# Performance work log

Measured on AMD Instinct MI355X. Metric: run time of the kernel, lower is better.

Reference implementation:

```python
import jax, jax.numpy as jnp
import numpy as np

N_NODES = 4096
D_FEAT = 256


def _interp_linear_2x(x):
    # Matches F.interpolate(mode='linear', scale_factor=2, align_corners=False)
    # applied along the node axis. x: [N, D] -> [2N, D]
    n = x.shape[0]
    out_i = jnp.arange(2 * n, dtype=jnp.float32)
    src = jnp.clip((out_i + 0.5) * 0.5 - 0.5, 0.0, float(n - 1))
    i0 = jnp.floor(src).astype(jnp.int32)
    i1 = jnp.minimum(i0 + 1, n - 1)
    w = (src - i0.astype(jnp.float32))[:, None]
    return x[i0] * (1.0 - w) + x[i1] * w


def _nearest_neighbor_idx(x):
    # argmin over pairwise Euclidean distances with diagonal excluded.
    # Squared distances give the same argmin as torch.cdist.
    sq = jnp.sum(x * x, axis=1)
    d2 = sq[:, None] + sq[None, :] - 2.0 * (x @ x.T)  # [2N, 2N]
    m = x.shape[0]
    d2 = jnp.where(jnp.eye(m, dtype=bool), jnp.inf, d2)
    return jnp.argmin(d2, axis=1)


def setup_inputs() -> dict:
    key = jax.random.key(0)
    k1, k2, k3, k4 = jax.random.split(key, 4)
    x = jax.random.normal(k1, (N_NODES, D_FEAT), dtype=jnp.float32)
    adj = jax.random.uniform(k2, (N_NODES, N_NODES), dtype=jnp.float32)
    # Xavier-uniform-ish init for the two GCN weights
    lim = float(np.sqrt(6.0 / (D_FEAT + D_FEAT)))
    W1 = jax.random.uniform(k3, (D_FEAT, D_FEAT), jnp.float32, -lim, lim)
    W2 = jax.random.uniform(k4, (D_FEAT, D_FEAT), jnp.float32, -lim, lim)
    return {"x": x, "adj": adj, "W1": W1, "W2": W2}


def reference(x, adj, W1, W2):
    # conv1: adj @ (x @ W1)
    h = adj @ (x @ W1)                      # [N, D]
    x2 = _interp_linear_2x(h)               # [2N, D]
    # nearest-neighbor one-hot adjacency, then conv2.
    # one_hot(nn_idx) @ support == support[nn_idx] (exact same math)
    nn_idx = _nearest_neighbor_idx(x2)      # [2N]
    support = x2 @ W2                       # [2N, D]
    return support[nn_idx]                  # [2N, D]
```

## Files before the change

### kernel.cpp

```cpp
#include <hip/hip_runtime.h>
#include <hip/hip_bf16.h>
#include <cstdint>

typedef __attribute__((ext_vector_type(8))) __bf16 bf16x8;
typedef __attribute__((ext_vector_type(4))) float f32x4;

static __device__ __forceinline__ unsigned short f2bf(float f) {
  return __builtin_bit_cast(unsigned short, (__bf16)f);
}
static __device__ __forceinline__ unsigned pack2(float a, float b) {
  return (unsigned)f2bf(a) | ((unsigned)f2bf(b) << 16);
}
#define GLDS(src, dst) __builtin_amdgcn_global_load_lds( \
    (const __attribute__((address_space(1))) void*)(src), \
    (__attribute__((address_space(3))) void*)(dst), 16, 0, 0)


__global__ void transpose_w_kernel(const float* __restrict__ W1, const float* __restrict__ W2,
                                   unsigned short* __restrict__ W1t, unsigned short* __restrict__ W2t) {
  int i = blockIdx.x * 256 + threadIdx.x;
  int k = i >> 8, n = i & 255;
  W1t[n * 256 + k] = f2bf(W1[k * 256 + n]);
  W2t[n * 256 + k] = f2bf(W2[k * 256 + n]);
}

__global__ void upsample_kernel(const unsigned short* __restrict__ hs,
                                unsigned short* __restrict__ x2b, float* __restrict__ sq) {
  int row = blockIdx.x * 4 + (threadIdx.x >> 6);
  int c = (threadIdx.x & 63) * 4;
  float s = (row + 0.5f) * 0.5f - 0.5f;
  s = fminf(fmaxf(s, 0.0f), 4095.0f);
  float fl = floorf(s);
  int i0 = (int)fl;
  int i1 = min((int)fl + 1, 4095);
  float w = s - fl;
  float v0[4] = {0.f, 0.f, 0.f, 0.f}, v1[4] = {0.f, 0.f, 0.f, 0.f};
  #pragma unroll
  for (int k = 0; k < 8; ++k) {
    ushort4 u0 = *(const ushort4*)&hs[(size_t)k * 4096 * 256 + i0 * 256 + c];
    ushort4 u1 = *(const ushort4*)&hs[(size_t)k * 4096 * 256 + i1 * 256 + c];
    v0[0] += __builtin_bit_cast(float, (unsigned)u0.x << 16);
    v0[1] += __builtin_bit_cast(float, (unsigned)u0.y << 16);
    v0[2] += __builtin_bit_cast(float, (unsigned)u0.z << 16);
    v0[3] += __builtin_bit_cast(float, (unsigned)u0.w << 16);
    v1[0] += __builtin_bit_cast(float, (unsigned)u1.x << 16);
    v1[1] += __builtin_bit_cast(float, (unsigned)u1.y << 16);
    v1[2] += __builtin_bit_cast(float, (unsigned)u1.z << 16);
    v1[3] += __builtin_bit_cast(float, (unsigned)u1.w << 16);
  }
  float p = 0.f;
  ushort4 st;
  unsigned short* sp = (unsigned short*)&st;
  #pragma unroll
  for (int e = 0; e < 4; ++e) {
    float v = v0[e] * (1.0f - w) + v1[e] * w;
    sp[e] = f2bf(v);
    p += v * v;
  }
  *(ushort4*)&x2b[(size_t)row * 256 + c] = st;
  #pragma unroll
  for (int m = 32; m > 0; m >>= 1) p += __shfl_down(p, m, 64);
  if ((threadIdx.x & 63) == 0) sq[row] = p;
}

__global__ void argmin_reduce_kernel(const unsigned* __restrict__ pv,
                                     unsigned* __restrict__ pck) {
  int row = blockIdx.x * 256 + threadIdx.x;
  int cr = row >> 7;
  unsigned best = 0xFFFFFFFFu;
  for (int c = 0; c <= cr; ++c) best = min(best, pv[(size_t)c * 8192 + row]);
  for (int c = cr + 1; c < 64; ++c) best = min(best, pv[(size_t)(64 + c) * 8192 + row]);
  pck[row] = best & 0x1FFFu;
}

__launch_bounds__(256, 3)
__global__ void gram_kernel(const unsigned short* __restrict__ X,
                            const float* __restrict__ sq,
                            unsigned* __restrict__ pv) {
  __shared__ alignas(16) unsigned short As[128 * 64];
  __shared__ alignas(16) unsigned short Bs[128 * 64];
  __shared__ unsigned mrgr[2][128];
  __shared__ unsigned mrgc[2][128];

  const int tid = threadIdx.x;
  const int wid = tid >> 6;
  const int lane = tid & 63;
  const int g = lane >> 4, lr = lane & 15;
  const int wr = wid >> 1, wc = wid & 1;

  int t = blockIdx.x;
  int bi = (int)((sqrtf(8.0f * (float)t + 1.0f) - 1.0f) * 0.5f);
  while ((bi + 1) * (bi + 2) / 2 <= t) ++bi;
  while (bi * (bi + 1) / 2 > t) --bi;
  const int bx = bi;
  const int by = t - bi * (bi + 1) / 2;
  const int m0 = bx * 128;
  const int n0 = by * 128;
  const bool diag = (bx == by);

  const int srow = tid >> 3;
  const int ssc = (tid & 7) ^ (srow & 7);
  const unsigned short* aBase = X + (size_t)(m0 + srow) * 256 + ssc * 8;
  const unsigned short* bBase = X + (size_t)(n0 + srow) * 256 + ssc * 8;
  unsigned short* const aDst = As + (size_t)(tid >> 6) * 512;
  unsigned short* const bDst = Bs + (size_t)(tid >> 6) * 512;
  const unsigned short* const Bsrc = diag ? As : Bs;

  f32x4 acc[4][4];
  const f32x4 fzero = {0.f, 0.f, 0.f, 0.f};
  #pragma unroll
  for (int i = 0; i < 4; ++i)
    #pragma unroll
    for (int j = 0; j < 4; ++j) acc[i][j] = fzero;

  #pragma unroll
  for (int ks = 0; ks < 4; ++ks) {
    #pragma unroll
    for (int it = 0; it < 4; ++it)
      GLDS(aBase + it * 8192 + ks * 64, aDst + it * 2048);
    if (!diag) {
      #pragma unroll
      for (int it = 0; it < 4; ++it)
        GLDS(bBase + it * 8192 + ks * 64, bDst + it * 2048);
    }
    __syncthreads();
    #pragma unroll
    for (int kk = 0; kk < 2; ++kk) {
      const int ch = (kk * 4 + g) ^ (lr & 7);
      bf16x8 b[4];
      #pragma unroll
      for (int j = 0; j < 4; ++j)
        b[j] = *(const bf16x8*)&Bsrc[(wc * 64 + j * 16 + lr) * 64 + ch * 8];
      #pragma unroll
      for (int i = 0; i < 4; ++i) {
        bf16x8 a = *(const bf16x8*)&As[(wr * 64 + i * 16 + lr) * 64 + ch * 8];
        #pragma unroll
        for (int j = 0; j < 4; ++j)
          acc[i][j] = __builtin_amdgcn_mfma_f32_16x16x32_bf16(a, b[j], acc[i][j], 0, 0, 0);
      }
    }
    __syncthreads();
  }

  int jcol[4];
  float sqj[4];
  unsigned ckey[4];
  #pragma unroll
  for (int j = 0; j < 4; ++j) {
    jcol[j] = n0 + wc * 64 + j * 16 + lr;
    sqj[j] = sq[jcol[j]];
    ckey[j] = 0xFFFFFFFFu;
  }
  #pragma unroll
  for (int i = 0; i < 4; ++i) {
    #pragma unroll
    for (int r = 0; r < 4; ++r) {
      const int lrow = wr * 64 + i * 16 + g * 4 + r;
      const int irow = m0 + lrow;
      const float sqi = sq[irow];
      unsigned rk = 0xFFFFFFFFu;
      #pragma unroll
      for (int j = 0; j < 4; ++j) {
        float v = fmaf(-2.0f, acc[i][j][r], sqi + sqj[j]);
        unsigned bits = __float_as_uint(v) & 0xFFFFE000u;
        unsigned krow = bits | (unsigned)jcol[j];
        if (diag && jcol[j] == irow) krow = 0xFFFFFFFFu;
        rk = min(rk, krow);
        if (!diag) ckey[j] = min(ckey[j], bits | (unsigned)irow);
      }
      #pragma unroll
      for (int m = 1; m < 16; m <<= 1)
        rk = min(rk, (unsigned)__shfl_xor((int)rk, m, 64));
      if (lr == 0) mrgr[wc][lrow] = rk;
    }
  }
  if (!diag) {
    #pragma unroll
    for (int j = 0; j < 4; ++j) {
      ckey[j] = min(ckey[j], (unsigned)__shfl_xor((int)ckey[j], 16, 64));
      ckey[j] = min(ckey[j], (unsigned)__shfl_xor((int)ckey[j], 32, 64));
      if (g == 0) mrgc[wr][wc * 64 + j * 16 + lr] = ckey[j];
    }
  }
  __syncthreads();
  if (tid < 128) {
    pv[(size_t)by * 8192 + m0 + tid] = min(mrgr[0][tid], mrgr[1][tid]);
  } else if (!diag) {
    int c = tid - 128;
    pv[(size_t)(64 + bx) * 8192 + n0 + c] = min(mrgc[0][c], mrgc[1][c]);
  }
}

template <int BM, int BN, int WAVES_M, int KT, int EPI, bool AF32, bool GATHER>
__launch_bounds__(256)
__global__ void gemm_nt_kernel(const void* __restrict__ Ap, int lda,
                               const unsigned short* __restrict__ Bp, int ldb,
                               int M, int N,
                               float* __restrict__ Cf,
                               unsigned short* __restrict__ Cb,
                               const unsigned* __restrict__ gidx) {
  constexpr int BK = 64;
  constexpr int NT = KT / BK;
  constexpr int WAVES_N = 4 / WAVES_M;
  constexpr int WM = BM / WAVES_M;
  constexpr int WN = BN / WAVES_N;
  constexpr int FM = WM / 16;
  constexpr int FN = WN / 16;
  constexpr int ASLOT = BM * 8;
  constexpr int AITER = (ASLOT + 255) / 256;
  constexpr int BITER = (BN * 8) / 256;

  __shared__ alignas(16) unsigned short As[BM * BK];
  __shared__ alignas(16) unsigned short Bs[BN * BK];

  const int tid = threadIdx.x;
  const int wid = tid >> 6;
  const int lane = tid & 63;
  const int g = lane >> 4;
  const int lr = lane & 15;
  const int wr = wid / WAVES_N;
  const int wc = wid % WAVES_N;
  const int m0 = blockIdx.x * BM;
  const int n0 = (EPI == 3) ? 0 : blockIdx.y * BN;
  const int kbase = (EPI == 3) ? blockIdx.y * KT : 0;
  if constexpr (EPI == 3) Cb += (size_t)blockIdx.y * (size_t)M * (size_t)N;

  const int srow = tid >> 3;
  const int ssc = (tid & 7) ^ (srow & 7);
  const float* aBF[AITER];
  const unsigned short* aBH[AITER];
  #pragma unroll
  for (int it = 0; it < AITER; ++it) {
    int r = m0 + srow + it * 32;
    if constexpr (AF32) {
      aBF[it] = (const float*)Ap + (size_t)r * (size_t)lda + kbase + ssc * 8;
    } else {
      int sr = GATHER ? (int)gidx[r] : r;
      aBH[it] = (const unsigned short*)Ap + (size_t)sr * (size_t)lda + kbase + ssc * 8;
    }
  }
  const unsigned short* bBase = Bp + (size_t)(n0 + srow) * (size_t)ldb + kbase + ssc * 8;
  unsigned short* const sDst = As + (size_t)wid * 512;
  unsigned short* const bDst = Bs + (size_t)wid * 512;

  f32x4 acc[FM][FN];
  const f32x4 fzero = {0.f, 0.f, 0.f, 0.f};
  #pragma unroll
  for (int i = 0; i < FM; ++i)
    #pragma unroll
    for (int j = 0; j < FN; ++j) acc[i][j] = fzero;

  #pragma unroll
  for (int t = 0; t < NT; ++t) {
    #pragma unroll
    for (int it = 0; it < BITER; ++it)
      GLDS(bBase + (size_t)it * 32 * ldb + t * 64, bDst + it * 2048);
    if constexpr (AF32) {
      #pragma unroll
      for (int it = 0; it < AITER; ++it) {
        if (ASLOT % 256 == 0 || it * 256 + tid < ASLOT) {
          const float* src = aBF[it] + t * 64;
          float4 f0 = *(const float4*)src;
          float4 f1 = *(const float4*)(src + 4);
          uint4 pk = { pack2(f0.x, f0.y), pack2(f0.z, f0.w),
                       pack2(f1.x, f1.y), pack2(f1.z, f1.w) };
          *(uint4*)&As[(it * 32 + srow) * BK + (tid & 7) * 8] = pk;
        }
      }
    } else {
      #pragma unroll
      for (int it = 0; it < AITER; ++it)
        GLDS(aBH[it] + t * 64, sDst + it * 2048);
    }
    __syncthreads();
    #pragma unroll
    for (int kk = 0; kk < 2; ++kk) {
      const int ch = (kk * 4 + g) ^ (lr & 7);
      bf16x8 a[FM], b[FN];
      #pragma unroll
      for (int i = 0; i < FM; ++i)
        a[i] = *(const bf16x8*)&As[(wr * WM + i * 16 + lr) * BK + ch * 8];
      #pragma unroll
      for (int j = 0; j < FN; ++j)
        b[j] = *(const bf16x8*)&Bs[(wc * WN + j * 16 + lr) * BK + ch * 8];
      #pragma unroll
      for (int i = 0; i < FM; ++i)
        #pragma unroll
        for (int j = 0; j < FN; ++j)
          acc[i][j] = __builtin_amdgcn_mfma_f32_16x16x32_bf16(a[i], b[j], acc[i][j], 0, 0, 0);
    }
    __syncthreads();
  }

  const int rowb = wr * WM;
  const int colb = wc * WN;
  if constexpr (EPI == 0) {
    #pragma unroll
    for (int i = 0; i < FM; ++i) {
      int mrow = m0 + rowb + i * 16 + g * 4;
      #pragma unroll
      for (int j = 0; j < FN; ++j) {
        int col = n0 + colb + j * 16 + lr;
        #pragma unroll
        for (int r = 0; r < 4; ++r)
          Cf[(size_t)(mrow + r) * N + col] = acc[i][j][r];
      }
    }
  } else if constexpr (EPI == 1) {
    #pragma unroll
    for (int i = 0; i < FM; ++i) {
      int mrow = m0 + rowb + i * 16 + g * 4;
      #pragma unroll
      for (int j = 0; j < FN; ++j) {
        int col = n0 + colb + j * 16 + lr;
        ushort4 st;
        st.x = f2bf(acc[i][j][0]);
        st.y = f2bf(acc[i][j][1]);
        st.z = f2bf(acc[i][j][2]);
        st.w = f2bf(acc[i][j][3]);
        *(ushort4*)&Cb[(size_t)col * M + mrow] = st;
      }
    }
  } else {
    #pragma unroll
    for (int i = 0; i < FM; ++i) {
      int mrow = m0 + rowb + i * 16 + g * 4;
      #pragma unroll
      for (int j = 0; j < FN; ++j) {
        int col = n0 + colb + j * 16 + lr;
        #pragma unroll
        for (int r = 0; r < 4; ++r)
          Cb[(size_t)(mrow + r) * N + col] = f2bf(acc[i][j][r]);
      }
    }
  }
}


extern "C" void kernel_launch(void* const* d_in, const int* in_sizes, int n_in,
                              void* d_out, int out_size, void* d_ws, size_t ws_size,
                              hipStream_t stream) {
  (void)in_sizes; (void)n_in; (void)out_size; (void)ws_size;
  const float* x   = (const float*)d_in[0];
  const float* adj = (const float*)d_in[1];
  const float* W1  = (const float*)d_in[2];
  const float* W2  = (const float*)d_in[3];
  float* out = (float*)d_out;

  char* p = (char*)d_ws;
  unsigned short* Tt  = (unsigned short*)p;  p += 4096 * 256 * 2;
  char* R             = p;                   p += 16 * 1024 * 1024;
  unsigned short* x2b = (unsigned short*)p;  p += 8192 * 256 * 2;
  float* sqv          = (float*)p;           p += 8192 * 4;
  unsigned* pck       = (unsigned*)p;        p += 8192 * 4;
  unsigned short* W1t = (unsigned short*)p;  p += 256 * 256 * 2;
  unsigned short* W2t = (unsigned short*)p;  p += 256 * 256 * 2;

  unsigned short* hs = (unsigned short*)R;
  unsigned* pv       = (unsigned*)R;

  transpose_w_kernel<<<256, 256, 0, stream>>>(W1, W2, W1t, W2t);

  gemm_nt_kernel<64, 64, 4, 256, 1, true, false><<<dim3(64, 4), 256, 0, stream>>>(
      x, 256, W1t, 256, 4096, 256, nullptr, Tt, nullptr);

  gemm_nt_kernel<64, 256, 1, 512, 3, true, false><<<dim3(64, 8), 256, 0, stream>>>(
      adj, 4096, Tt, 4096, 4096, 256, nullptr, hs, nullptr);

  upsample_kernel<<<2048, 256, 0, stream>>>(hs, x2b, sqv);

  gram_kernel<<<2080, 256, 0, stream>>>(x2b, sqv, pv);

  argmin_reduce_kernel<<<32, 256, 0, stream>>>(pv, pck);

  gemm_nt_kernel<64, 64, 4, 256, 0, false, true><<<dim3(128, 4), 256, 0, stream>>>(
      x2b, 256, W2t, 256, 8192, 256, out, nullptr, pck);
}
```

Baseline: 98.03 us.

## Add dedicated double-buffered split-K kernel for adjacency GEMM

Replaces the generic gemm template instantiation for adj @ (x W1) with a specialized kernel that double-buffers both A and B tiles in LDS. It prefetches the next fp32 adj tile into registers and issues async global-to-LDS loads for the next Tt tile while MFMAs run on the current buffer. Explicit waitcnt and barriers replace the per-iteration __syncthreads. The split-K EPI==3 path is removed from the generic template. This doubles LDS use per block, which may lower occupancy.

```diff
diff --git a/kernel.cpp b/kernel.cpp
--- a/kernel.cpp
+++ b/kernel.cpp
@@ -71,6 +71,109 @@
   for (int c = 0; c <= cr; ++c) best = min(best, pv[(size_t)c * 8192 + row]);
   for (int c = cr + 1; c < 64; ++c) best = min(best, pv[(size_t)(64 + c) * 8192 + row]);
   pck[row] = best & 0x1FFFu;
+}
+
+__launch_bounds__(256)
+__global__ void adj_gemm_kernel(const float* __restrict__ adjp,
+                                const unsigned short* __restrict__ Ttp,
+                                unsigned short* __restrict__ hs) {
+  constexpr int NT = 8;
+  __shared__ alignas(16) unsigned short As[2][64 * 64];
+  __shared__ alignas(16) unsigned short Bs[2][256 * 64];
+
+  const int tid = threadIdx.x;
+  const int wid = tid >> 6;
+  const int lane = tid & 63;
+  const int g = lane >> 4, lr = lane & 15;
+  const int m0 = blockIdx.x * 64;
+  const int kbase = blockIdx.y * 512;
+  unsigned short* outp = hs + (size_t)blockIdx.y * 4096 * 256;
+
+  const int srow = tid >> 3;
+  const int scp = tid & 7;
+  const int ssc = scp ^ (srow & 7);
+  const float* aBase0 = adjp + (size_t)(m0 + srow) * 4096 + kbase + ssc * 8;
+  const float* aBase1 = aBase0 + (size_t)32 * 4096;
+  const unsigned short* bBase = Ttp + (size_t)srow * 4096 + kbase + ssc * 8;
+
+  f32x4 acc[4][4];
+  const f32x4 fzero = {0.f, 0.f, 0.f, 0.f};
+  #pragma unroll
+  for (int i = 0; i < 4; ++i)
+    #pragma unroll
+    for (int j = 0; j < 4; ++j) acc[i][j] = fzero;
+
+  float4 ar[2][2];
+  auto loadA = [&](int t) {
+    #pragma unroll
+    for (int it = 0; it < 2; ++it) {
+      const float* s = (it ? aBase1 : aBase0) + t * 64;
+      ar[it][0] = *(const float4*)s;
+      ar[it][1] = *(const float4*)(s + 4);
+    }
+  };
+  auto writeA = [&](int buf) {
+    #pragma unroll
+    for (int it = 0; it < 2; ++it) {
+      uint4 pk = { pack2(ar[it][0].x, ar[it][0].y), pack2(ar[it][0].z, ar[it][0].w),
+                   pack2(ar[it][1].x, ar[it][1].y), pack2(ar[it][1].z, ar[it][1].w) };
+      *(uint4*)&As[buf][(it * 32 + srow) * 64 + scp * 8] = pk;
+    }
+  };
+  auto stageB = [&](int t, int buf) {
+    #pragma unroll
+    for (int it = 0; it < 8; ++it)
+      GLDS(bBase + (size_t)it * 32 * 4096 + t * 64, Bs[buf] + ((size_t)it * 256 + wid * 64) * 8);
+  };
+
+  loadA(0);
+  stageB(0, 0);
+  writeA(0);
+
+  #pragma unroll
+  for (int t = 0; t < NT; ++t) {
+    const int cur = t & 1;
+    if (t + 1 < NT) {
+      loadA(t + 1);
+      stageB(t + 1, cur ^ 1);
+      asm volatile("s_waitcnt vmcnt(12) lgkmcnt(0)" ::: "memory");
+    } else {
+      asm volatile("s_waitcnt vmcnt(0) lgkmcnt(0)" ::: "memory");
+    }
+    __builtin_amdgcn_sched_barrier(0);
+    __builtin_amdgcn_s_barrier();
+    __builtin_amdgcn_sched_barrier(0);
+    #pragma unroll
+    for (int kk = 0; kk < 2; ++kk) {
+      const int ch = (kk * 4 + g) ^ (lr & 7);
+      bf16x8 a[4], b[4];
+      #pragma unroll
+      for (int i = 0; i < 4; ++i)
+        a[i] = *(const bf16x8*)&As[cur][(i * 16 + lr) * 64 + ch * 8];
+      #pragma unroll
+      for (int j = 0; j < 4; ++j)
+        b[j] = *(const bf16x8*)&Bs[cur][(wid * 64 + j * 16 + lr) * 64 + ch * 8];
+      #pragma unroll
+      for (int i = 0; i < 4; ++i)
+        #pragma unroll
+        for (int j = 0; j < 4; ++j)
+          acc[i][j] = __builtin_amdgcn_mfma_f32_16x16x32_bf16(a[i], b[j], acc[i][j], 0, 0, 0);
+    }
+    __builtin_amdgcn_s_barrier();
+    if (t + 1 < NT) writeA(cur ^ 1);
+  }
+
+  #pragma unroll
+  for (int i = 0; i < 4; ++i) {
+    int mrow = m0 + i * 16 + g * 4;
+    #pragma unroll
+    for (int j = 0; j < 4; ++j) {
+      int col = wid * 64 + j * 16 + lr;
+      #pragma unroll
+      for (int r = 0; r < 4; ++r)
+        outp[(size_t)(mrow + r) * 256 + col] = f2bf(acc[i][j][r]);
+    }
+  }
 }
 
 __launch_bounds__(256, 3)
@@ -221,9 +324,8 @@
   const int wr = wid / WAVES_N;
   const int wc = wid % WAVES_N;
   const int m0 = blockIdx.x * BM;
-  const int n0 = (EPI == 3) ? 0 : blockIdx.y * BN;
-  const int kbase = (EPI == 3) ? blockIdx.y * KT : 0;
-  if constexpr (EPI == 3) Cb += (size_t)blockIdx.y * (size_t)M * (size_t)N;
+  const int n0 = blockIdx.y * BN;
+  constexpr int kbase = 0;
 
   const int srow = tid >> 3;
   const int ssc = (tid & 7) ^ (srow & 7);
@@ -306,7 +408,7 @@
           Cf[(size_t)(mrow + r) * N + col] = acc[i][j][r];
       }
     }
-  } else if constexpr (EPI == 1) {
+  } else {
     #pragma unroll
     for (int i = 0; i < FM; ++i) {
       int mrow = m0 + rowb + i * 16 + g * 4;
@@ -321,18 +423,6 @@
         *(ushort4*)&Cb[(size_t)col * M + mrow] = st;
       }
     }
-  } else {
-    #pragma unroll
-    for (int i = 0; i < FM; ++i) {
-      int mrow = m0 + rowb + i * 16 + g * 4;
-      #pragma unroll
-      for (int j = 0; j < FN; ++j) {
-        int col = n0 + colb + j * 16 + lr;
-        #pragma unroll
-        for (int r = 0; r < 4; ++r)
-          Cb[(size_t)(mrow + r) * N + col] = f2bf(acc[i][j][r]);
-      }
-    }
   }
 }
 
@@ -364,8 +454,7 @@
   gemm_nt_kernel<64, 64, 4, 256, 1, true, false><<<dim3(64, 4), 256, 0, stream>>>(
       x, 256, W1t, 256, 4096, 256, nullptr, Tt, nullptr);
 
-  gemm_nt_kernel<64, 256, 1, 512, 3, true, false><<<dim3(64, 8), 256, 0, stream>>>(
-      adj, 4096, Tt, 4096, 4096, 256, nullptr, hs, nullptr);
+  adj_gemm_kernel<<<dim3(64, 8), 256, 0, stream>>>(adj, Tt, hs);
 
   upsample_kernel<<<2048, 256, 0, stream>>>(hs, x2b, sqv);
 
```

Result: no change. 98.19 us (+0.2%).

## Fuse argmin reduction into gather GEMM and retile adj GEMM to 128x128

Applied to the files above, without the earlier changes.

Removes the separate argmin_reduce kernel. Each gather-GEMM block now reduces the per-column-tile partial minima for its 64 rows into shared memory before loading its A rows, which saves one launch and one global round trip. Each row's reduction is repeated across the 4 N-blocks, adding some redundant reads of pv. Separately, the split-K adj GEMM moves from 64x256 tiles on a 2D grid to 128x128 tiles on a 3D grid (z indexes the K split), which changes data reuse and block count.

```diff
diff --git a/kernel.cpp b/kernel.cpp
--- a/kernel.cpp
+++ b/kernel.cpp
@@ -63,16 +63,6 @@
   if ((threadIdx.x & 63) == 0) sq[row] = p;
 }
 
-__global__ void argmin_reduce_kernel(const unsigned* __restrict__ pv,
-                                     unsigned* __restrict__ pck) {
-  int row = blockIdx.x * 256 + threadIdx.x;
-  int cr = row >> 7;
-  unsigned best = 0xFFFFFFFFu;
-  for (int c = 0; c <= cr; ++c) best = min(best, pv[(size_t)c * 8192 + row]);
-  for (int c = cr + 1; c < 64; ++c) best = min(best, pv[(size_t)(64 + c) * 8192 + row]);
-  pck[row] = best & 0x1FFFu;
-}
-
 __launch_bounds__(256, 3)
 __global__ void gram_kernel(const unsigned short* __restrict__ X,
                             const float* __restrict__ sq,
@@ -198,7 +188,7 @@
                                int M, int N,
                                float* __restrict__ Cf,
                                unsigned short* __restrict__ Cb,
-                               const unsigned* __restrict__ gidx) {
+                               const unsigned* __restrict__ pv) {
   constexpr int BK = 64;
   constexpr int NT = KT / BK;
   constexpr int WAVES_N = 4 / WAVES_M;
@@ -212,6 +202,8 @@
 
   __shared__ alignas(16) unsigned short As[BM * BK];
   __shared__ alignas(16) unsigned short Bs[BN * BK];
+  __shared__ unsigned redp[GATHER ? 4 * 64 : 1];
+  __shared__ unsigned pckl[GATHER ? 64 : 1];
 
   const int tid = threadIdx.x;
   const int wid = tid >> 6;
@@ -221,9 +213,29 @@
   const int wr = wid / WAVES_N;
   const int wc = wid % WAVES_N;
   const int m0 = blockIdx.x * BM;
-  const int n0 = (EPI == 3) ? 0 : blockIdx.y * BN;
-  const int kbase = (EPI == 3) ? blockIdx.y * KT : 0;
-  if constexpr (EPI == 3) Cb += (size_t)blockIdx.y * (size_t)M * (size_t)N;
+  const int n0 = blockIdx.y * BN;
+  const int kbase = (EPI == 3) ? blockIdx.z * KT : 0;
+  if constexpr (EPI == 3) Cb += (size_t)blockIdx.z * (size_t)M * (size_t)N;
+
+  if constexpr (GATHER) {
+    static_assert(!GATHER || BM == 64, "inline reduce assumes BM==64");
+    const int row = tid & 63;
+    const int part = tid >> 6;
+    const int cr = m0 >> 7;
+    unsigned best = 0xFFFFFFFFu;
+    #pragma unroll
+    for (int s8 = 0; s8 < 16; ++s8) {
+      int s = part * 16 + s8;
+      int slot = s + (s > cr ? 64 : 0);
+      best = min(best, pv[(size_t)slot * 8192 + m0 + row]);
+    }
+    redp[part * 64 + row] = best;
+    __syncthreads();
+    if (tid < 64)
+      pckl[tid] = min(min(redp[tid], redp[64 + tid]),
+                      min(redp[128 + tid], redp[192 + tid])) & 0x1FFFu;
+    __syncthreads();
+  }
 
   const int srow = tid >> 3;
   const int ssc = (tid & 7) ^ (srow & 7);
@@ -235,7 +247,7 @@
     if constexpr (AF32) {
       aBF[it] = (const float*)Ap + (size_t)r * (size_t)lda + kbase + ssc * 8;
     } else {
-      int sr = GATHER ? (int)gidx[r] : r;
+      int sr = GATHER ? (int)pckl[srow + it * 32] : r;
       aBH[it] = (const unsigned short*)Ap + (size_t)sr * (size_t)lda + kbase + ssc * 8;
     }
   }
@@ -352,7 +364,6 @@
   char* R             = p;                   p += 16 * 1024 * 1024;
   unsigned short* x2b = (unsigned short*)p;  p += 8192 * 256 * 2;
   float* sqv          = (float*)p;           p += 8192 * 4;
-  unsigned* pck       = (unsigned*)p;        p += 8192 * 4;
   unsigned short* W1t = (unsigned short*)p;  p += 256 * 256 * 2;
   unsigned short* W2t = (unsigned short*)p;  p += 256 * 256 * 2;
 
@@ -364,15 +375,13 @@
   gemm_nt_kernel<64, 64, 4, 256, 1, true, false><<<dim3(64, 4), 256, 0, stream>>>(
       x, 256, W1t, 256, 4096, 256, nullptr, Tt, nullptr);
 
-  gemm_nt_kernel<64, 256, 1, 512, 3, true, false><<<dim3(64, 8), 256, 0, stream>>>(
+  gemm_nt_kernel<128, 128, 2, 512, 3, true, false><<<dim3(32, 2, 8), 256, 0, stream>>>(
       adj, 4096, Tt, 4096, 4096, 256, nullptr, hs, nullptr);
 
   upsample_kernel<<<2048, 256, 0, stream>>>(hs, x2b, sqv);
 
   gram_kernel<<<2080, 256, 0, stream>>>(x2b, sqv, pv);
 
-  argmin_reduce_kernel<<<32, 256, 0, stream>>>(pv, pck);
-
   gemm_nt_kernel<64, 64, 4, 256, 0, false, true><<<dim3(128, 4), 256, 0, stream>>>(
-      x2b, 256, W2t, 256, 8192, 256, out, nullptr, pck);
-}
+      x2b, 256, W2t, 256, 8192, 256, out, nullptr, pv);
+}
```

After: 89.65 us. -8.5%, faster.
